# Kernel optimization log

Measured on AMD Instinct MI355X. Metric: run time of the kernel, lower is better.

Reference implementation:

```python
import jax, jax.numpy as jnp
import numpy as np
from jax import lax

D_MODEL = 1024
D_INNER = 2048   # expand * d_model
D_STATE = 16
DT_RANK = 64     # ceil(d_model / 16)
D_CONV = 4
B, L = 2, 1024


def setup_inputs() -> dict:
    key = jax.random.key(0)
    ks = jax.random.split(key, 8)
    s = 0.02
    x = jax.random.normal(ks[0], (B, L, D_MODEL), dtype=jnp.float32)
    in_proj_w = jax.random.normal(ks[1], (2 * D_INNER, D_MODEL), dtype=jnp.float32) * s
    conv_w = jax.random.normal(ks[2], (D_INNER, D_CONV), dtype=jnp.float32) * s  # depthwise kernel
    conv_b = jax.random.normal(ks[3], (D_INNER,), dtype=jnp.float32) * s
    x_proj_w = jax.random.normal(ks[4], (DT_RANK + 2 * D_STATE, D_INNER), dtype=jnp.float32) * s
    dt_proj_w = jax.random.normal(ks[5], (D_INNER, DT_RANK), dtype=jnp.float32) * s
    dt_proj_b = jax.random.normal(ks[6], (D_INNER,), dtype=jnp.float32) * s
    A_log = jnp.log(jnp.broadcast_to(jnp.arange(1, D_STATE + 1, dtype=jnp.float32), (D_INNER, D_STATE)))
    D = jnp.ones((D_INNER,), dtype=jnp.float32)
    out_proj_w = jax.random.normal(ks[7], (D_MODEL, D_INNER), dtype=jnp.float32) * s
    return {"x": x, "in_proj_w": in_proj_w, "conv_w": conv_w, "conv_b": conv_b,
            "x_proj_w": x_proj_w, "dt_proj_w": dt_proj_w, "dt_proj_b": dt_proj_b,
            "A_log": A_log, "D": D, "out_proj_w": out_proj_w}


def _causal_depthwise_conv(x, conv_w, conv_b):
    # x: (B, L, d_inner); torch Conv1d(padding=d_conv-1) then [:, :, :L] == causal left pad
    Lx = x.shape[1]
    k = conv_w.shape[-1]
    xp = jnp.pad(x, ((0, 0), (k - 1, 0), (0, 0)))
    out = conv_b
    # small fixed kernel width (4): unrolled taps, fully vectorized over B,L,D
    out = sum(xp[:, i:i + Lx, :] * conv_w[:, i] for i in range(k)) + conv_b
    return out


def mamba_forward(x, in_proj_w, conv_w, conv_b, x_proj_w, dt_proj_w, dt_proj_b, A_log, D, out_proj_w):
    xz = x @ in_proj_w.T                       # (B, L, 2*d_inner)
    xi, z = xz[..., :D_INNER], xz[..., D_INNER:]
    xc = jax.nn.silu(_causal_depthwise_conv(xi, conv_w, conv_b))  # (B, L, d_inner)

    x_dbl = xc @ x_proj_w.T                    # (B, L, dt_rank + 2*d_state)
    dt = x_dbl[..., :DT_RANK]
    Bm = x_dbl[..., DT_RANK:DT_RANK + D_STATE]  # (B, L, N)
    Cm = x_dbl[..., DT_RANK + D_STATE:]         # (B, L, N)
    delta = jax.nn.softplus(dt @ dt_proj_w.T + dt_proj_b)  # (B, L, d_inner)

    A = -jnp.exp(A_log)                        # (d_inner, N)
    deltaA = jnp.exp(delta[..., None] * A)                           # (B, L, D, N)
    deltaBx = delta[..., None] * Bm[:, :, None, :] * xc[..., None]   # (B, L, D, N)

    def step(h, inp):
        dA, dBx, Ct = inp                      # (B,D,N), (B,D,N), (B,N)
        h = dA * h + dBx
        y = jnp.einsum('bdn,bn->bd', h, Ct)
        return h, y

    h0 = jnp.zeros((x.shape[0], D_INNER, D_STATE), dtype=x.dtype)
    _, ys = lax.scan(step, h0, (deltaA.transpose(1, 0, 2, 3),
                                deltaBx.transpose(1, 0, 2, 3),
                                Cm.transpose(1, 0, 2)))
    y = ys.transpose(1, 0, 2)                  # (B, L, d_inner)
    y = y + xc * D
    y = y * jax.nn.silu(z)
    return y @ out_proj_w.T                    # (B, L, d_model)


def reference(x, in_proj_w, conv_w, conv_b, x_proj_w, dt_proj_w, dt_proj_b, A_log, D, out_proj_w):
    return mamba_forward(x, in_proj_w, conv_w, conv_b, x_proj_w, dt_proj_w, dt_proj_b, A_log, D, out_proj_w)
```

## Files before the change

kernel.cpp:

```cpp
#include <hip/hip_runtime.h>
#include <hip/hip_bf16.h>
#include <cstdint>
#include <cstddef>

#define DMODEL 1024
#define DINNER 2048
#define NSTATE 16
#define DTRANK 64
#define BATCH 2
#define SEQ 1024
#define ROWS (BATCH*SEQ)
#define NCHUNK 32
#define CLEN (SEQ/NCHUNK)
#define KSPLIT 16

typedef __attribute__((ext_vector_type(8))) short short8;
typedef __attribute__((ext_vector_type(4))) short short4v;
typedef __attribute__((ext_vector_type(4))) float f32x4;

__device__ __forceinline__ float bf2f(__hip_bfloat16 h){ return __bfloat162float(h); }
__device__ __forceinline__ float sigmoidf_(float x){ return 1.0f/(1.0f + __expf(-x)); }
__device__ __forceinline__ unsigned short f2bfbits(float v){
  __hip_bfloat16 h = __float2bfloat16(v);
  return *(unsigned short*)&h;
}
__device__ __forceinline__ float bfbits2f(unsigned short u){
  unsigned int x = ((unsigned int)u) << 16;
  return *(float*)&x;
}

__device__ __forceinline__ void gld16(const void* g, void* l){
  __builtin_amdgcn_global_load_lds((const __attribute__((address_space(1))) void*)g,
                                   (__attribute__((address_space(3))) void*)l, 16, 0, 0);
}

__global__ void sniff_k(const unsigned short* __restrict__ xu, int* __restrict__ flag)
{
  int t = threadIdx.x;
  int cnt = 0;
  for (int i = t; i < 1024; i += 64) {
    unsigned short u = xu[i];
    int e = (u >> 7) & 0xFF;
    if (e >= 0x70 && e <= 0x86) cnt++;
  }
  for (int o = 32; o; o >>= 1) cnt += __shfl_down(cnt, o);
  if (t == 0) *flag = (cnt >= 768) ? 0 : 1;
}

struct CvtArgs {
  const void *s0,*s1,*s2,*s3,*s4,*s5,*s6,*s7,*s8,*s9;
  __hip_bfloat16 *xB,*inpB,*xprojB,*dtprojB,*outpB;
  float *cwF,*cbF,*dtbF,*alF,*DF;
  float *xdblZ;
  const int* flag;
};
#define CVT_C1 2097152
#define CVT_C2 6291456
#define CVT_C3 6299648
#define CVT_C4 6301696
#define CVT_C5 6498304
#define CVT_C6 6629376
#define CVT_C7 6631424
#define CVT_C8 6664192
#define CVT_C9 6666240
#define CVT_TOT 8763392
#define CVT_BLOCKS (CVT_TOT/4/256)

__device__ __forceinline__ void cvt_read4(const void* s, int j, int fl, float v[4]){
  if (fl) {
    f32x4 t = ((const f32x4*)s)[j>>2];
    v[0]=t.x; v[1]=t.y; v[2]=t.z; v[3]=t.w;
  } else {
    short4v t = *(const short4v*)((const __hip_bfloat16*)s + j);
    v[0]=bfbits2f((unsigned short)t.x); v[1]=bfbits2f((unsigned short)t.y);
    v[2]=bfbits2f((unsigned short)t.z); v[3]=bfbits2f((unsigned short)t.w);
  }
}
__device__ __forceinline__ void cvt_wB(__hip_bfloat16* d, int j, const float v[4]){
  short4v o;
  o.x=(short)f2bfbits(v[0]); o.y=(short)f2bfbits(v[1]);
  o.z=(short)f2bfbits(v[2]); o.w=(short)f2bfbits(v[3]);
  *(short4v*)(d + j) = o;
}
__device__ __forceinline__ void cvt_wF(float* d, int j, const float v[4]){
  f32x4 o = { v[0], v[1], v[2], v[3] };
  *(f32x4*)(d + j) = o;
}

__global__ __launch_bounds__(256)
void convert_all_k(CvtArgs a)
{
  int i4 = blockIdx.x * 256 + threadIdx.x;
  const int fl = *a.flag;

  if (blockIdx.x < 192) {
    f32x4 z = {0.f, 0.f, 0.f, 0.f};
    ((f32x4*)a.xdblZ)[i4] = z;
  }

  int i = i4 * 4;
  if (i >= CVT_TOT) return;
  float v[4];
  if (i < CVT_C1)      { cvt_read4(a.s0, i, fl, v);        cvt_wB(a.xB, i, v); }
  else if (i < CVT_C2) { cvt_read4(a.s1, i-CVT_C1, fl, v); cvt_wB(a.inpB, i-CVT_C1, v); }
  else if (i < CVT_C3) { cvt_read4(a.s2, i-CVT_C2, fl, v); cvt_wF(a.cwF, i-CVT_C2, v); }
  else if (i < CVT_C4) { cvt_read4(a.s3, i-CVT_C3, fl, v); cvt_wF(a.cbF, i-CVT_C3, v); }
  else if (i < CVT_C5) { cvt_read4(a.s4, i-CVT_C4, fl, v); cvt_wB(a.xprojB, i-CVT_C4, v); }
  else if (i < CVT_C6) { cvt_read4(a.s5, i-CVT_C5, fl, v); cvt_wB(a.dtprojB, i-CVT_C5, v); }
  else if (i < CVT_C7) { cvt_read4(a.s6, i-CVT_C6, fl, v); cvt_wF(a.dtbF, i-CVT_C6, v); }
  else if (i < CVT_C8) { cvt_read4(a.s7, i-CVT_C7, fl, v); cvt_wF(a.alF, i-CVT_C7, v); }
  else if (i < CVT_C9) { cvt_read4(a.s8, i-CVT_C8, fl, v); cvt_wF(a.DF, i-CVT_C8, v); }
  else                 { cvt_read4(a.s9, i-CVT_C9, fl, v); cvt_wB(a.outpB, i-CVT_C9, v); }
}

template<int EPI>
__global__ __launch_bounds__(256)
void gemm64(const __hip_bfloat16* __restrict__ A,
            const __hip_bfloat16* __restrict__ W,
            int M, int N, int K, int kchunk,
            float* __restrict__ outF,
            __hip_bfloat16* __restrict__ outH,
            __hip_bfloat16* __restrict__ outH2,
            const float* __restrict__ biasF,
            float* __restrict__ q0, float* __restrict__ q1,
            float* __restrict__ q2, float* __restrict__ q3)
{
  __shared__ alignas(16) __hip_bfloat16 As[128*64];
  __shared__ alignas(16) __hip_bfloat16 Ws[128*64];
  const int tid  = threadIdx.x;
  const int lane = tid & 63;
  const int wave = tid >> 6;
  const int wm = wave & 1, wn = wave >> 1;
  const int row0 = blockIdx.y * 128;
  const int col0 = blockIdx.x * 128;

  f32x4 acc[4][4] = {};

  int kbeg = 0, kend = K;
  if (EPI == 5 || EPI == 6) { kbeg = blockIdx.z * kchunk; kend = kbeg + kchunk; }

  const int r16 = lane & 15, q = lane >> 4;
  const int sx0 = ((q ^ (r16 & 7)) * 16);

  for (int k0 = kbeg; k0 < kend; k0 += 64) {
#pragma unroll
    for (int j = 0; j < 4; ++j) {
      int e = tid + j*256;
      int r = e >> 3, g = e & 7;
      int kc = ((g ^ (r & 7)) << 3);
      gld16(A + (size_t)(row0 + r) * K + k0 + kc, (char*)As + (size_t)e*16);
    }
#pragma unroll
    for (int j = 0; j < 4; ++j) {
      int e = tid + j*256;
      int r = e >> 3, g = e & 7;
      int kc = ((g ^ (r & 7)) << 3);
      int rw = col0 + r; if (EPI == 5 && rw > N-1) rw = N-1;
      gld16(W + (size_t)rw * K + k0 + kc, (char*)Ws + (size_t)e*16);
    }
    __syncthreads();

    const char* Ab = (const char*)As + ((wm*64 + r16) * 128);
    const char* Wb = (const char*)Ws + ((wn*64 + r16) * 128);
#pragma unroll
    for (int ksub = 0; ksub < 2; ++ksub) {
      const int sx = sx0 ^ (ksub * 64);
      short8 af[4], wf[4];
#pragma unroll
      for (int i = 0; i < 4; ++i) af[i] = *(const short8*)(Ab + i*16*128 + sx);
#pragma unroll
      for (int i = 0; i < 4; ++i) wf[i] = *(const short8*)(Wb + i*16*128 + sx);
#pragma unroll
      for (int mt = 0; mt < 4; ++mt)
#pragma unroll
        for (int nt = 0; nt < 4; ++nt)
          acc[mt][nt] = __builtin_amdgcn_mfma_f32_16x16x32_bf16(af[mt], wf[nt], acc[mt][nt], 0, 0, 0);
    }
    __syncthreads();
  }

  const int mbase = row0 + wm*64 + (q * 4);
  const int nbase = col0 + wn*64 + r16;

  float bv[4];
  if (EPI == 3) {
#pragma unroll
    for (int nt = 0; nt < 4; ++nt) bv[nt] = biasF[nbase + nt*16];
  }
  float* qz = nullptr;
  if (EPI == 6) qz = (blockIdx.z == 0) ? q0 : (blockIdx.z == 1) ? q1
                   : (blockIdx.z == 2) ? q2 : q3;

#pragma unroll
  for (int mt = 0; mt < 4; ++mt) {
#pragma unroll
    for (int nt = 0; nt < 4; ++nt) {
#pragma unroll
      for (int r = 0; r < 4; ++r) {
        int row = mbase + mt*16 + r;
        int col = nbase + nt*16;
        float v = acc[mt][nt][r];
        if (EPI == 3) {
          v += bv[nt];
          float sp = fmaxf(v, 0.0f) + __logf(1.0f + __expf(-fabsf(v)));
          outF[(size_t)row * DINNER + col] = sp;
        } else if (EPI == 4) {
          if (col < DINNER) {
            outH[(size_t)row * DINNER + col] = __float2bfloat16(v);
          } else {
            outH2[(size_t)row * DINNER + (col - DINNER)] = __float2bfloat16(v * sigmoidf_(v));
          }
        } else if (EPI == 5) {
          if (col < 96)
            unsafeAtomicAdd(&outF[(size_t)row * 96 + col], v);
        } else if (EPI == 6) {
          qz[(size_t)row * DMODEL + col] = v;
        }
      }
    }
  }
}

__global__ __launch_bounds__(256)
void reduce_out_k(const float* __restrict__ q0, const float* __restrict__ q1,
                  const float* __restrict__ q2, const float* __restrict__ q3,
                  float* __restrict__ out)
{
  int i4 = blockIdx.x * 256 + threadIdx.x;
  if (i4 >= ROWS*DMODEL/4) return;
  f32x4 a = ((const f32x4*)q0)[i4];
  f32x4 b = ((const f32x4*)q1)[i4];
  f32x4 c = ((const f32x4*)q2)[i4];
  f32x4 d = ((const f32x4*)q3)[i4];
  f32x4 o = { (a.x+b.x)+(c.x+d.x), (a.y+b.y)+(c.y+d.y),
              (a.z+b.z)+(c.z+d.z), (a.w+b.w)+(c.w+d.w) };
  ((f32x4*)out)[i4] = o;
}

__global__ __launch_bounds__(256)
void dt_cvt_k(const float* __restrict__ xdbl, __hip_bfloat16* __restrict__ dtH)
{
  int i = blockIdx.x * 256 + threadIdx.x;
  if (i >= ROWS*64) return;
  int row = i >> 6, col = i & 63;
  dtH[i] = __float2bfloat16(xdbl[(size_t)row*96 + col]);
}

__global__ __launch_bounds__(256)
void conv_silu_k(const __hip_bfloat16* __restrict__ xi,
                 const float* __restrict__ cw,
                 const float* __restrict__ cb,
                 __hip_bfloat16* __restrict__ xcH)
{
  int idx4 = blockIdx.x * 256 + threadIdx.x;
  int idx  = idx4 * 4;
  int d  = idx & (DINNER - 1);
  int t  = (idx >> 11) & (SEQ - 1);
  int bt = idx >> 11;

  f32x4 cb4 = *(const f32x4*)&cb[d];
  float a0=cb4.x, a1=cb4.y, a2=cb4.z, a3=cb4.w;
  f32x4 w0 = *(const f32x4*)&cw[(d+0)*4];
  f32x4 w1 = *(const f32x4*)&cw[(d+1)*4];
  f32x4 w2 = *(const f32x4*)&cw[(d+2)*4];
  f32x4 w3 = *(const f32x4*)&cw[(d+3)*4];

#pragma unroll
  for (int i = 0; i < 4; ++i) {
    if (t - 3 + i >= 0) {
      short4v xv = *(const short4v*)(xi + (size_t)(bt - 3 + i) * DINNER + d);
      float x0 = bfbits2f((unsigned short)xv.x);
      float x1 = bfbits2f((unsigned short)xv.y);
      float x2 = bfbits2f((unsigned short)xv.z);
      float x3 = bfbits2f((unsigned short)xv.w);
      float c0 = (i==0)?w0.x:(i==1)?w0.y:(i==2)?w0.z:w0.w;
      float c1 = (i==0)?w1.x:(i==1)?w1.y:(i==2)?w1.z:w1.w;
      float c2 = (i==0)?w2.x:(i==1)?w2.y:(i==2)?w2.z:w2.w;
      float c3 = (i==0)?w3.x:(i==1)?w3.y:(i==2)?w3.z:w3.w;
      a0 += c0*x0; a1 += c1*x1; a2 += c2*x2; a3 += c3*x3;
    }
  }
  float y0 = a0 * sigmoidf_(a0);
  float y1 = a1 * sigmoidf_(a1);
  float y2 = a2 * sigmoidf_(a2);
  float y3 = a3 * sigmoidf_(a3);
  short4v o;
  o.x=(short)f2bfbits(y0); o.y=(short)f2bfbits(y1);
  o.z=(short)f2bfbits(y2); o.w=(short)f2bfbits(y3);
  *(short4v*)(xcH + idx) = o;
}

#define GSTEP 8

__global__ __launch_bounds__(256)
void stats_k(const float* __restrict__ delta,
             const __hip_bfloat16* __restrict__ xcH,
             const float* __restrict__ xdbl,
             const float* __restrict__ alF,
             float* __restrict__ Hc, float* __restrict__ Sd)
{
  __shared__ alignas(16) float Bs[CLEN*16];
  const int bid  = blockIdx.x;
  const int b    = bid >> 10;
  const int c    = (bid >> 5) & (NCHUNK-1);
  const int cg   = bid & 31;
  const int tid  = threadIdx.x;
  const int lane = tid & 63;
  const int wave = tid >> 6;
  const int sub  = lane & 3;
  const int ch   = (cg << 6) + (wave << 4) + (lane >> 2);

  const size_t rb = (size_t)b * SEQ + (size_t)c * CLEN;

  for (int i = tid; i < CLEN*16; i += 256) {
    int t = i >> 4, j = i & 15;
    Bs[i] = xdbl[(rb + t)*96 + 64 + j];
  }
  __syncthreads();

  float negA[4];
#pragma unroll
  for (int j = 0; j < 4; ++j) negA[j] = -__expf(alF[ch*NSTATE + sub*4 + j]);

  const float*          dp = delta + rb * DINNER + ch;
  const __hip_bfloat16* xp = xcH   + rb * DINNER + ch;

  float h0=0.f,h1=0.f,h2=0.f,h3=0.f, sd=0.f;
  float d0[GSTEP], x0[GSTEP], d1[GSTEP], x1[GSTEP];

#define PF1(D_,X_,T0) \
  _Pragma("unroll") \
  for (int u = 0; u < GSTEP; ++u) { \
    D_[u] = dp[(size_t)((T0)+u) * DINNER]; \
    X_[u] = bf2f(xp[(size_t)((T0)+u) * DINNER]); \
  }
#define ST1(D_,X_,T0) \
  _Pragma("unroll") \
  for (int u = 0; u < GSTEP; ++u) { \
    float d_ = D_[u]; \
    sd += d_; \
    float du = d_ * X_[u]; \
    f32x4 B4 = *(const f32x4*)&Bs[((T0)+u)*16 + sub*4]; \
    h0 = __expf(d_*negA[0])*h0 + du*B4.x; \
    h1 = __expf(d_*negA[1])*h1 + du*B4.y; \
    h2 = __expf(d_*negA[2])*h2 + du*B4.z; \
    h3 = __expf(d_*negA[3])*h3 + du*B4.w; \
  }

  PF1(d0, x0, 0)
  for (int t0 = 0; t0 < CLEN; t0 += 2*GSTEP) {
    PF1(d1, x1, t0 + GSTEP)
    ST1(d0, x0, t0)
    if (t0 + 2*GSTEP < CLEN) { PF1(d0, x0, t0 + 2*GSTEP) }
    ST1(d1, x1, t0 + GSTEP)
  }
#undef PF1
#undef ST1

  const size_t bc = (size_t)(b*NCHUNK + c);
  f32x4 hv = { h0, h1, h2, h3 };
  *(f32x4*)&Hc[(bc*DINNER + ch)*NSTATE + sub*4] = hv;
  if (sub == 0) Sd[bc*DINNER + ch] = sd;
}

__global__ __launch_bounds__(256)
void carry_k(const float* __restrict__ Hc, const float* __restrict__ Sd,
             const float* __restrict__ alF, float* __restrict__ hin)
{
  int i = blockIdx.x * 256 + threadIdx.x;
  int n  = i & (NSTATE-1);
  int ch = (i >> 4) & (DINNER-1);
  int b  = i >> 15;
  float negA = -__expf(alF[ch * NSTATE + n]);
  float h = 0.f;
#pragma unroll
  for (int c = 0; c < NCHUNK; ++c) {
    size_t bc = (size_t)(b*NCHUNK + c);
    hin[(bc*DINNER + ch)*NSTATE + n] = h;
    float P = __expf(negA * Sd[bc*DINNER + ch]);
    h = P * h + Hc[(bc*DINNER + ch)*NSTATE + n];
  }
}

__global__ __launch_bounds__(256)
void emit_k(const float* __restrict__ delta,
            const __hip_bfloat16* __restrict__ xcH,
            const float* __restrict__ xdbl,
            const __hip_bfloat16* __restrict__ zsH,
            const float* __restrict__ alF,
            const float* __restrict__ DF,
            const float* __restrict__ hin,
            __hip_bfloat16* __restrict__ yH)
{
  __shared__ alignas(16) float BCs[CLEN*32];
  const int bid  = blockIdx.x;
  const int b    = bid >> 10;
  const int c    = (bid >> 5) & (NCHUNK-1);
  const int cg   = bid & 31;
  const int tid  = threadIdx.x;
  const int lane = tid & 63;
  const int wave = tid >> 6;
  const int sub  = lane & 3;
  const int ch   = (cg << 6) + (wave << 4) + (lane >> 2);

  const size_t rb = (size_t)b * SEQ + (size_t)c * CLEN;

  for (int i = tid; i < CLEN*32; i += 256) {
    int t = i >> 5, j = i & 31;
    BCs[i] = xdbl[(rb + t)*96 + 64 + j];
  }
  __syncthreads();

  float negA[4];
#pragma unroll
  for (int j = 0; j < 4; ++j) negA[j] = -__expf(alF[ch*NSTATE + sub*4 + j]);
  const float Dch = DF[ch];

  const float*          dp = delta + rb * DINNER + ch;
  const __hip_bfloat16* xp = xcH   + rb * DINNER + ch;
  const __hip_bfloat16* zp = zsH   + rb * DINNER + ch;
  __hip_bfloat16*       yp = yH    + rb * DINNER + ch;

  f32x4 hv = *(const f32x4*)&hin[((size_t)(b*NCHUNK + c)*DINNER + ch)*NSTATE + sub*4];
  float h0=hv.x, h1=hv.y, h2=hv.z, h3=hv.w;

  float d0[GSTEP], x0[GSTEP], z0[GSTEP], d1[GSTEP], x1[GSTEP], z1[GSTEP];

#define PF(D_,X_,Z_,T0) \
  _Pragma("unroll") \
  for (int u = 0; u < GSTEP; ++u) { \
    D_[u] = dp[(size_t)((T0)+u) * DINNER]; \
    X_[u] = bf2f(xp[(size_t)((T0)+u) * DINNER]); \
    Z_[u] = bf2f(zp[(size_t)((T0)+u) * DINNER]); \
  }
#define STEPS(D_,X_,Z_,T0) \
  _Pragma("unroll") \
  for (int u = 0; u < GSTEP; ++u) { \
    float d_ = D_[u]; \
    float du = d_ * X_[u]; \
    f32x4 B4 = *(const f32x4*)&BCs[((T0)+u)*32 + sub*4]; \
    f32x4 C4 = *(const f32x4*)&BCs[((T0)+u)*32 + 16 + sub*4]; \
    h0 = __expf(d_*negA[0])*h0 + du*B4.x; \
    h1 = __expf(d_*negA[1])*h1 + du*B4.y; \
    h2 = __expf(d_*negA[2])*h2 + du*B4.z; \
    h3 = __expf(d_*negA[3])*h3 + du*B4.w; \
    float p = h0*C4.x + h1*C4.y + h2*C4.z + h3*C4.w; \
    p += __shfl_xor(p, 1); \
    p += __shfl_xor(p, 2); \
    if (sub == 0) { \
      float y = (p + X_[u] * Dch) * Z_[u]; \
      yp[(size_t)((T0)+u) * DINNER] = __float2bfloat16(y); \
    } \
  }

  PF(d0, x0, z0, 0)
  for (int t0 = 0; t0 < CLEN; t0 += 2*GSTEP) {
    PF(d1, x1, z1, t0 + GSTEP)
    STEPS(d0, x0, z0, t0)
    if (t0 + 2*GSTEP < CLEN) { PF(d0, x0, z0, t0 + 2*GSTEP) }
    STEPS(d1, x1, z1, t0 + GSTEP)
  }
#undef PF
#undef STEPS
}

extern "C" void kernel_launch(void* const* d_in, const int* in_sizes, int n_in,
                              void* d_out, int out_size, void* d_ws, size_t ws_size,
                              hipStream_t stream)
{
  float* out = (float*)d_out;
  char* ws = (char*)d_ws;
  const size_t MB = 1024*1024;

  int*            flag    = (int*)            (ws);
  float*          cwF     = (float*)          (ws + 1024);
  float*          cbF     = (float*)          (ws + 40*1024);
  float*          dtbF    = (float*)          (ws + 56*1024);
  float*          alF     = (float*)          (ws + 72*1024);
  float*          DF      = (float*)          (ws + 208*1024);
  float*          Sd      = (float*)          (ws + 256*1024);
  __hip_bfloat16* xB      = (__hip_bfloat16*) (ws + 1*MB);
  __hip_bfloat16* inpB    = (__hip_bfloat16*) (ws + 5*MB);
  __hip_bfloat16* xiB     = (__hip_bfloat16*) (ws + 13*MB);
  float*          dlt     = (float*)          (ws + 1*MB);
  __hip_bfloat16* xprojB  = (__hip_bfloat16*) (ws + 21*MB);
  __hip_bfloat16* dtprojB = (__hip_bfloat16*) (ws + 21*MB + 512*1024);
  __hip_bfloat16* outpB   = (__hip_bfloat16*) (ws + 22*MB);
  __hip_bfloat16* zsH     = (__hip_bfloat16*) (ws + 26*MB);
  __hip_bfloat16* xcH     = (__hip_bfloat16*) (ws + 42*MB);
  float*          xdbl    = (float*)          (ws + 50*MB);
  __hip_bfloat16* dtH     = (__hip_bfloat16*) (ws + 51*MB);
  __hip_bfloat16* yH      = (__hip_bfloat16*) (ws + 52*MB);
  float*          Hc      = (float*)          (ws + 68*MB);
  float*          hin     = (float*)          (ws + 76*MB);
  float*          q0      = (float*)          (ws + 1*MB);
  float*          q1      = (float*)          (ws + 9*MB);
  float*          q2      = (float*)          (ws + 26*MB);
  float*          q3      = (float*)          (ws + 34*MB);

  dim3 blk(256);

  sniff_k<<<1, 64, 0, stream>>>((const unsigned short*)d_in[0], flag);
  CvtArgs ca = { d_in[0], d_in[1], d_in[2], d_in[3], d_in[4],
                 d_in[5], d_in[6], d_in[7], d_in[8], d_in[9],
                 xB, inpB, xprojB, dtprojB, outpB,
                 cwF, cbF, dtbF, alF, DF, xdbl, flag };
  convert_all_k<<<CVT_BLOCKS, blk, 0, stream>>>(ca);

  gemm64<4><<<dim3(4096/128, ROWS/128), blk, 0, stream>>>(
      xB, inpB, ROWS, 2*DINNER, DMODEL, 0, nullptr, xiB, zsH, nullptr,
      nullptr, nullptr, nullptr, nullptr);

  conv_silu_k<<<(ROWS*DINNER/4)/256, blk, 0, stream>>>(xiB, cwF, cbF, xcH);

  gemm64<5><<<dim3(1, ROWS/128, KSPLIT), blk, 0, stream>>>(
      xcH, xprojB, ROWS, 96, DINNER, DINNER/KSPLIT, xdbl, nullptr, nullptr, nullptr,
      nullptr, nullptr, nullptr, nullptr);
  dt_cvt_k<<<(ROWS*64)/256, blk, 0, stream>>>(xdbl, dtH);

  gemm64<3><<<dim3(DINNER/128, ROWS/128), blk, 0, stream>>>(
      dtH, dtprojB, ROWS, DINNER, DTRANK, 0, dlt, nullptr, nullptr, dtbF,
      nullptr, nullptr, nullptr, nullptr);

  stats_k<<<BATCH*NCHUNK*32, blk, 0, stream>>>(dlt, xcH, xdbl, alF, Hc, Sd);
  carry_k<<<(BATCH*DINNER*NSTATE)/256, blk, 0, stream>>>(Hc, Sd, alF, hin);
  emit_k<<<BATCH*NCHUNK*32, blk, 0, stream>>>(dlt, xcH, xdbl, zsH, alF, DF, hin, yH);

  gemm64<6><<<dim3(DMODEL/128, ROWS/128, 4), blk, 0, stream>>>(
      yH, outpB, ROWS, DMODEL, DINNER, DINNER/4, nullptr, nullptr, nullptr, nullptr,
      q0, q1, q2, q3);
  reduce_out_k<<<(ROWS*DMODEL/4)/256, blk, 0, stream>>>(q0, q1, q2, q3, out);
}
```

Baseline: 232.4 us.

## Switch GEMMs to 32x32x16 MFMA and fuse split-K reduction via last-block counter

The GEMM inner loop now uses 32x32x16 bf16 MFMA tiles (2x2 per wave) instead of 16x16x32 (4x4), which cuts the number of LDS fragment loads and MFMA issues per k-step. For the output projection, the separate reduce kernel is removed. Each tile instead bumps an atomic counter, and the last of the four split-K blocks sums the partial buffers and writes the output. This saves a launch and a full pass over the output, at the cost of threadfence/atomic synchronisation and a serialized tail reduction in one block per tile.

```diff
diff --git a/kernel.cpp b/kernel.cpp
--- a/kernel.cpp
+++ b/kernel.cpp
@@ -17,6 +17,7 @@
 typedef __attribute__((ext_vector_type(8))) short short8;
 typedef __attribute__((ext_vector_type(4))) short short4v;
 typedef __attribute__((ext_vector_type(4))) float f32x4;
+typedef __attribute__((ext_vector_type(16))) float f32x16;
 
 __device__ __forceinline__ float bf2f(__hip_bfloat16 h){ return __bfloat162float(h); }
 __device__ __forceinline__ float sigmoidf_(float x){ return 1.0f/(1.0f + __expf(-x)); }
@@ -52,6 +53,7 @@
   __hip_bfloat16 *xB,*inpB,*xprojB,*dtprojB,*outpB;
   float *cwF,*cbF,*dtbF,*alF,*DF;
   float *xdblZ;
+  unsigned *cnt;
   const int* flag;
 };
 #define CVT_C1 2097152
@@ -97,6 +99,9 @@
     f32x4 z = {0.f, 0.f, 0.f, 0.f};
     ((f32x4*)a.xdblZ)[i4] = z;
   }
+  if (blockIdx.x == 0 && threadIdx.x < 128) {
+    a.cnt[threadIdx.x] = 0u;
+  }
 
   int i = i4 * 4;
   if (i >= CVT_TOT) return;
@@ -123,7 +128,8 @@
             __hip_bfloat16* __restrict__ outH2,
             const float* __restrict__ biasF,
             float* __restrict__ q0, float* __restrict__ q1,
-            float* __restrict__ q2, float* __restrict__ q3)
+            float* __restrict__ q2, float* __restrict__ q3,
+            unsigned* __restrict__ cnt)
 {
   __shared__ alignas(16) __hip_bfloat16 As[128*64];
   __shared__ alignas(16) __hip_bfloat16 Ws[128*64];
@@ -134,13 +140,14 @@
   const int row0 = blockIdx.y * 128;
   const int col0 = blockIdx.x * 128;
 
-  f32x4 acc[4][4] = {};
+  f32x16 acc[2][2] = {};
 
   int kbeg = 0, kend = K;
   if (EPI == 5 || EPI == 6) { kbeg = blockIdx.z * kchunk; kend = kbeg + kchunk; }
 
-  const int r16 = lane & 15, q = lane >> 4;
-  const int sx0 = ((q ^ (r16 & 7)) * 16);
+  const int r32   = lane & 31;
+  const int khalf = lane >> 5;
+  const int swz   = r32 & 7;
 
   for (int k0 = kbeg; k0 < kend; k0 += 64) {
 #pragma unroll
@@ -160,45 +167,40 @@
     }
     __syncthreads();
 
-    const char* Ab = (const char*)As + ((wm*64 + r16) * 128);
-    const char* Wb = (const char*)Ws + ((wn*64 + r16) * 128);
-#pragma unroll
-    for (int ksub = 0; ksub < 2; ++ksub) {
-      const int sx = sx0 ^ (ksub * 64);
-      short8 af[4], wf[4];
-#pragma unroll
-      for (int i = 0; i < 4; ++i) af[i] = *(const short8*)(Ab + i*16*128 + sx);
-#pragma unroll
-      for (int i = 0; i < 4; ++i) wf[i] = *(const short8*)(Wb + i*16*128 + sx);
-#pragma unroll
-      for (int mt = 0; mt < 4; ++mt)
-#pragma unroll
-        for (int nt = 0; nt < 4; ++nt)
-          acc[mt][nt] = __builtin_amdgcn_mfma_f32_16x16x32_bf16(af[mt], wf[nt], acc[mt][nt], 0, 0, 0);
+    const char* Ab = (const char*)As + ((wm*64 + r32) * 128);
+    const char* Wb = (const char*)Ws + ((wn*64 + r32) * 128);
+#pragma unroll
+    for (int ks = 0; ks < 4; ++ks) {
+      const int sx = (((ks*2 + khalf) ^ swz) * 16);
+      short8 a0 = *(const short8*)(Ab + sx);
+      short8 a1 = *(const short8*)(Ab + 32*128 + sx);
+      short8 w0 = *(const short8*)(Wb + sx);
+      short8 w1 = *(const short8*)(Wb + 32*128 + sx);
+      acc[0][0] = __builtin_amdgcn_mfma_f32_32x32x16_bf16(a0, w0, acc[0][0], 0, 0, 0);
+      acc[0][1] = __builtin_amdgcn_mfma_f32_32x32x16_bf16(a0, w1, acc[0][1], 0, 0, 0);
+      acc[1][0] = __builtin_amdgcn_mfma_f32_32x32x16_bf16(a1, w0, acc[1][0], 0, 0, 0);
+      acc[1][1] = __builtin_amdgcn_mfma_f32_32x32x16_bf16(a1, w1, acc[1][1], 0, 0, 0);
     }
     __syncthreads();
   }
 
-  const int mbase = row0 + wm*64 + (q * 4);
-  const int nbase = col0 + wn*64 + r16;
-
-  float bv[4];
-  if (EPI == 3) {
-#pragma unroll
-    for (int nt = 0; nt < 4; ++nt) bv[nt] = biasF[nbase + nt*16];
-  }
+  const int mbase = row0 + wm*64 + 4*khalf;
+  const int nbase = col0 + wn*64 + r32;
+
+  float bv[2];
+  if (EPI == 3) { bv[0] = biasF[nbase]; bv[1] = biasF[nbase + 32]; }
   float* qz = nullptr;
   if (EPI == 6) qz = (blockIdx.z == 0) ? q0 : (blockIdx.z == 1) ? q1
                    : (blockIdx.z == 2) ? q2 : q3;
 
 #pragma unroll
-  for (int mt = 0; mt < 4; ++mt) {
-#pragma unroll
-    for (int nt = 0; nt < 4; ++nt) {
-#pragma unroll
-      for (int r = 0; r < 4; ++r) {
-        int row = mbase + mt*16 + r;
-        int col = nbase + nt*16;
+  for (int mt = 0; mt < 2; ++mt) {
+#pragma unroll
+    for (int nt = 0; nt < 2; ++nt) {
+#pragma unroll
+      for (int r = 0; r < 16; ++r) {
+        int row = mbase + mt*32 + (r & 3) + 8*(r >> 2);
+        int col = nbase + nt*32;
         float v = acc[mt][nt][r];
         if (EPI == 3) {
           v += bv[nt];
@@ -219,22 +221,32 @@
       }
     }
   }
-}
-
-__global__ __launch_bounds__(256)
-void reduce_out_k(const float* __restrict__ q0, const float* __restrict__ q1,
-                  const float* __restrict__ q2, const float* __restrict__ q3,
-                  float* __restrict__ out)
-{
-  int i4 = blockIdx.x * 256 + threadIdx.x;
-  if (i4 >= ROWS*DMODEL/4) return;
-  f32x4 a = ((const f32x4*)q0)[i4];
-  f32x4 b = ((const f32x4*)q1)[i4];
-  f32x4 c = ((const f32x4*)q2)[i4];
-  f32x4 d = ((const f32x4*)q3)[i4];
-  f32x4 o = { (a.x+b.x)+(c.x+d.x), (a.y+b.y)+(c.y+d.y),
-              (a.z+b.z)+(c.z+d.z), (a.w+b.w)+(c.w+d.w) };
-  ((f32x4*)out)[i4] = o;
+
+  if (EPI == 6) {
+    __shared__ unsigned sOld;
+    __threadfence();
+    __syncthreads();
+    if (tid == 0)
+      sOld = atomicAdd(&cnt[blockIdx.y * gridDim.x + blockIdx.x], 1u);
+    __syncthreads();
+    if (sOld == 3u) {
+      __threadfence();
+#pragma unroll
+      for (int i = 0; i < 16; ++i) {
+        int idx = tid + i*256;
+        int rr = idx >> 5;
+        int cc = (idx & 31) << 2;
+        size_t off = ((size_t)(row0 + rr) * DMODEL + col0 + cc) >> 2;
+        f32x4 a = ((const f32x4*)q0)[off];
+        f32x4 b = ((const f32x4*)q1)[off];
+        f32x4 c = ((const f32x4*)q2)[off];
+        f32x4 d = ((const f32x4*)q3)[off];
+        f32x4 o = { (a.x+b.x)+(c.x+d.x), (a.y+b.y)+(c.y+d.y),
+                    (a.z+b.z)+(c.z+d.z), (a.w+b.w)+(c.w+d.w) };
+        ((f32x4*)outF)[off] = o;
+      }
+    }
+  }
 }
 
 __global__ __launch_bounds__(256)
@@ -479,6 +491,7 @@
   float*          alF     = (float*)          (ws + 72*1024);
   float*          DF      = (float*)          (ws + 208*1024);
   float*          Sd      = (float*)          (ws + 256*1024);
+  unsigned*       cnt     = (unsigned*)       (ws + 768*1024);
   __hip_bfloat16* xB      = (__hip_bfloat16*) (ws + 1*MB);
   __hip_bfloat16* inpB    = (__hip_bfloat16*) (ws + 5*MB);
   __hip_bfloat16* xiB     = (__hip_bfloat16*) (ws + 13*MB);
@@ -504,30 +517,29 @@
   CvtArgs ca = { d_in[0], d_in[1], d_in[2], d_in[3], d_in[4],
                  d_in[5], d_in[6], d_in[7], d_in[8], d_in[9],
                  xB, inpB, xprojB, dtprojB, outpB,
-                 cwF, cbF, dtbF, alF, DF, xdbl, flag };
+                 cwF, cbF, dtbF, alF, DF, xdbl, cnt, flag };
   convert_all_k<<<CVT_BLOCKS, blk, 0, stream>>>(ca);
 
   gemm64<4><<<dim3(4096/128, ROWS/128), blk, 0, stream>>>(
       xB, inpB, ROWS, 2*DINNER, DMODEL, 0, nullptr, xiB, zsH, nullptr,
-      nullptr, nullptr, nullptr, nullptr);
+      nullptr, nullptr, nullptr, nullptr, nullptr);
 
   conv_silu_k<<<(ROWS*DINNER/4)/256, blk, 0, stream>>>(xiB, cwF, cbF, xcH);
 
   gemm64<5><<<dim3(1, ROWS/128, KSPLIT), blk, 0, stream>>>(
       xcH, xprojB, ROWS, 96, DINNER, DINNER/KSPLIT, xdbl, nullptr, nullptr, nullptr,
-      nullptr, nullptr, nullptr, nullptr);
+      nullptr, nullptr, nullptr, nullptr, nullptr);
   dt_cvt_k<<<(ROWS*64)/256, blk, 0, stream>>>(xdbl, dtH);
 
   gemm64<3><<<dim3(DINNER/128, ROWS/128), blk, 0, stream>>>(
       dtH, dtprojB, ROWS, DINNER, DTRANK, 0, dlt, nullptr, nullptr, dtbF,
-      nullptr, nullptr, nullptr, nullptr);
+      nullptr, nullptr, nullptr, nullptr, nullptr);
 
   stats_k<<<BATCH*NCHUNK*32, blk, 0, stream>>>(dlt, xcH, xdbl, alF, Hc, Sd);
   carry_k<<<(BATCH*DINNER*NSTATE)/256, blk, 0, stream>>>(Hc, Sd, alF, hin);
   emit_k<<<BATCH*NCHUNK*32, blk, 0, stream>>>(dlt, xcH, xdbl, zsH, alF, DF, hin, yH);
 
   gemm64<6><<<dim3(DMODEL/128, ROWS/128, 4), blk, 0, stream>>>(
-      yH, outpB, ROWS, DMODEL, DINNER, DINNER/4, nullptr, nullptr, nullptr, nullptr,
-      q0, q1, q2, q3);
-  reduce_out_k<<<(ROWS*DMODEL/4)/256, blk, 0, stream>>>(q0, q1, q2, q3, out);
-}
+      yH, outpB, ROWS, DMODEL, DINNER, DINNER/4, out, nullptr, nullptr, nullptr,
+      q0, q1, q2, q3, cnt);
+}
```

Result: slower. 307.4 us (+32.3%).
